# Performance work log

Hardware: AMD Instinct MI355X
Metric: run time of the kernel (lower is better)

Reference implementation:

```python
import jax, jax.numpy as jnp
import numpy as np

B, C_IN, C_OUT, H, W = 16, 64, 64, 256, 256
M1, M2 = 32, 32  # retained Fourier modes (low-frequency corner block)


def setup_inputs() -> dict:
    key = jax.random.key(0)
    kx, kw, kb = jax.random.split(key, 3)
    x = jax.random.normal(kx, (B, C_IN, H, W), dtype=jnp.float32)
    # xavier_uniform over (in, out, m1, m2): fan_in = C_IN*M1*M2, fan_out = C_OUT*M1*M2
    bound = float(np.sqrt(6.0 / ((C_IN + C_OUT) * M1 * M2)))
    weights = jax.random.uniform(kw, (C_IN, C_OUT, M1, M2), jnp.float32, -bound, bound)
    bias = jax.random.normal(kb, (C_OUT,), dtype=jnp.float32) * 0.01
    return {"x": x, "weights": weights, "bias": bias}


def reference(x, weights, bias):
    # x: [B, Cin, H, W] real -> rFFT2 -> [B, Cin, H, W//2+1] complex
    x_ft = jnp.fft.rfft2(x, axes=(-2, -1))
    m1 = min(M1, x_ft.shape[-2])
    m2 = min(M2, x_ft.shape[-1])
    # Single fused complex-times-real channel mixing over the truncated mode block
    mixed = jnp.einsum("bixy,ioxy->boxy",
                       x_ft[:, :, :m1, :m2],
                       weights[:, :, :m1, :m2].astype(x_ft.dtype))
    out_ft = jnp.zeros((x.shape[0], weights.shape[1], x_ft.shape[-2], x_ft.shape[-1]),
                       dtype=x_ft.dtype)
    out_ft = out_ft.at[:, :, :m1, :m2].set(mixed)
    x_out = jnp.fft.irfft2(out_ft, s=(x.shape[-2], x.shape[-1]), axes=(-2, -1))
    return x_out + bias[None, :, None, None]
```

## Files before the change

### kernel.cpp

```cpp
#include <hip/hip_runtime.h>


#define H_ 256
#define W_ 256

typedef short short8 __attribute__((ext_vector_type(8)));
typedef float floatx4 __attribute__((ext_vector_type(4)));

static __device__ __forceinline__ unsigned short f2b(float f) {
    union { float f; unsigned int u; } v; v.f = f;
    unsigned int r = v.u + 0x7FFFu + ((v.u >> 16) & 1u);
    return (unsigned short)(r >> 16);
}

__global__ void build_tables(unsigned short* ws) {
    int k = blockIdx.x;
    int n = threadIdx.x;
    int u = (k * n) & 255;
    double ang = 6.283185307179586476925286766559 * (double)u / 256.0;
    float c = (float)cos(ang), s = (float)sin(ang);
    unsigned short bc = f2b(c), bs = f2b(s), bns = f2b(-s);
    unsigned short* F2t = ws;
    unsigned short* F1e = ws + 16384;
    unsigned short* G1  = ws + 16384 + 32768;
    unsigned short* G2t = ws + 16384 + 65536;

    F2t[(2 * k) * 256 + n]     = bc;
    F2t[(2 * k + 1) * 256 + n] = bns;
    F1e[(2 * k) * 512 + 2 * n]         = bc;
    F1e[(2 * k) * 512 + 2 * n + 1]     = bs;
    F1e[(2 * k + 1) * 512 + 2 * n]     = bns;
    F1e[(2 * k + 1) * 512 + 2 * n + 1] = bc;
    G1[(2 * n) * 64 + 2 * k]         = bc;
    G1[(2 * n) * 64 + 2 * k + 1]     = bns;
    G1[(2 * n + 1) * 64 + 2 * k]     = bs;
    G1[(2 * n + 1) * 64 + 2 * k + 1] = bc;
    float fac = (k == 0) ? 1.f : 2.f;
    G2t[n * 64 + 2 * k]     = f2b(fac * c);
    G2t[n * 64 + 2 * k + 1] = f2b(-fac * s);
}

__global__ __launch_bounds__(256) void fwd_kernel(const float* __restrict__ x,
                                                  const unsigned short* __restrict__ ws_u,
                                                  float* __restrict__ Y) {
    __shared__ __align__(16) unsigned short lT[32 * 520];
    const int tid = threadIdx.x;
    const int wave = tid >> 6, lane = tid & 63;
    const int lm = lane & 15, lq = lane >> 4;
    const int bi = blockIdx.x;

    const float* xg = x + (size_t)bi * (H_ * W_);
    const unsigned short* F2tg = ws_u;
    const unsigned short* F1eg = ws_u + 16384;

    floatx4 acc[4][4];
    for (int a = 0; a < 4; ++a)
        for (int b = 0; b < 4; ++b) acc[a][b] = (floatx4){0.f, 0.f, 0.f, 0.f};

    for (int kc = 0; kc < 4; ++kc) {
        for (int kk = 0; kk < 2; ++kk) {
            short8 af[4], bf[4];
            for (int a = 0; a < 4; ++a) {
                const float* ap = xg + (((wave * 4 + a) * 16 + lm) * 256 + kc * 64 + kk * 32 + lq * 8);
                const float4 v0 = *(const float4*)ap;
                const float4 v1 = *(const float4*)(ap + 4);
                short8 t;
                t[0] = (short)f2b(v0.x); t[1] = (short)f2b(v0.y);
                t[2] = (short)f2b(v0.z); t[3] = (short)f2b(v0.w);
                t[4] = (short)f2b(v1.x); t[5] = (short)f2b(v1.y);
                t[6] = (short)f2b(v1.z); t[7] = (short)f2b(v1.w);
                af[a] = t;
            }
            for (int b = 0; b < 4; ++b)
                bf[b] = *(const short8*)(F2tg + (b * 16 + lm) * 256 + kc * 64 + kk * 32 + lq * 8);
            for (int a = 0; a < 4; ++a)
                for (int b = 0; b < 4; ++b)
                    acc[a][b] = __builtin_amdgcn_mfma_f32_16x16x32_bf16(af[a], bf[b], acc[a][b], 0, 0, 0);
        }
    }
    for (int a = 0; a < 4; ++a) {
        int mbase = (wave * 4 + a) * 16 + lq * 4;
        for (int b = 0; b < 4; ++b) {
            int col = b * 16 + lm;
            int ky = col >> 1, c = col & 1;
            for (int r = 0; r < 4; ++r) {
                int h = mbase + r;
                lT[ky * 520 + 2 * h + c] = f2b(acc[a][b][r]);
            }
        }
    }
    __syncthreads();
    floatx4 acc2[2];
    acc2[0] = (floatx4){0.f, 0.f, 0.f, 0.f};
    acc2[1] = (floatx4){0.f, 0.f, 0.f, 0.f};
    for (int ks = 0; ks < 16; ++ks) {
        short8 af = *(const short8*)(F1eg + (wave * 16 + lm) * 512 + ks * 32 + lq * 8);
        for (int b = 0; b < 2; ++b) {
            short8 bf = *(const short8*)(lT + (b * 16 + lm) * 520 + ks * 32 + lq * 8);
            acc2[b] = __builtin_amdgcn_mfma_f32_16x16x32_bf16(af, bf, acc2[b], 0, 0, 0);
        }
    }
    float* Yg = Y + (size_t)bi * (64 * 32);
    for (int b = 0; b < 2; ++b) {
        int colk = b * 16 + lm;
        int mrow = wave * 16 + lq * 4;
        for (int r = 0; r < 4; ++r)
            Yg[(mrow + r) * 32 + colk] = acc2[b][r];
    }
}

__global__ __launch_bounds__(256) void mix_kernel(const float* __restrict__ Wg,
                                                  const float* __restrict__ Y,
                                                  unsigned short* __restrict__ Mx) {
    __shared__ float lW[64 * 64];
    __shared__ float lY[16 * 130];
    const int tid = threadIdx.x;
    const int bid = blockIdx.x;
    const int mode = (bid & 7) * 128 + (bid >> 3);
    const int kx = mode >> 5, ky = mode & 31;

    for (int q = 0; q < 16; ++q) {
        int e = q * 256 + tid;
        lW[e] = Wg[(size_t)e * 1024 + kx * 32 + ky];
    }
    for (int q = 0; q < 8; ++q) {
        int e = q * 256 + tid;
        int b = e >> 7, r = e & 127;
        lY[b * 130 + r] = Y[(((size_t)b * 64 + (r >> 1)) * 64 + 2 * kx + (r & 1)) * 32 + ky];
    }
    __syncthreads();

    const int og = tid & 7;
    const int bc = tid >> 3;
    const int b = bc >> 1, c = bc & 1;
    float acc[8];
    for (int j = 0; j < 8; ++j) acc[j] = 0.f;
    for (int i = 0; i < 64; ++i) {
        float yv = lY[b * 130 + 2 * i + c];
        const floatx4 w0 = *(const floatx4*)&lW[i * 64 + og * 8];
        const floatx4 w1 = *(const floatx4*)&lW[i * 64 + og * 8 + 4];
        acc[0] += yv * w0[0]; acc[1] += yv * w0[1];
        acc[2] += yv * w0[2]; acc[3] += yv * w0[3];
        acc[4] += yv * w1[0]; acc[5] += yv * w1[1];
        acc[6] += yv * w1[2]; acc[7] += yv * w1[3];
    }
    const float scale = 1.f / 65536.f;
    for (int j = 0; j < 8; ++j) {
        int o = og * 8 + j;
        Mx[((size_t)(b * 64 + o) * 64 + 2 * kx + c) * 32 + ky] = f2b(acc[j] * scale);
    }
}

__global__ __launch_bounds__(256) void inv_kernel(const unsigned short* __restrict__ ws_u,
                                                  const unsigned short* __restrict__ Mx,
                                                  const float* __restrict__ bias,
                                                  float* __restrict__ out) {
    __shared__ __align__(16) unsigned short lMx[32 * 64];
    __shared__ __align__(16) unsigned short lZ[256 * 72];
    const int tid = threadIdx.x;
    const int wave = tid >> 6, lane = tid & 63;
    const int lm = lane & 15, lq = lane >> 4;
    const int bo = blockIdx.x;
    const int o = bo & 63;

    const unsigned short* G1g = ws_u + 49152;
    const unsigned short* G2g = ws_u + 81920;

    {
        short8 v = *(const short8*)(Mx + (size_t)bo * 2048 + tid * 8);
        int kx2 = tid >> 2, kyb = (tid & 3) * 8;
        for (int e = 0; e < 8; ++e)
            lMx[(kyb + e) * 64 + kx2] = (unsigned short)v[e];
    }
    __syncthreads();

    {
        floatx4 accc[8][2];
        for (int a = 0; a < 8; ++a)
            for (int b = 0; b < 2; ++b) accc[a][b] = (floatx4){0.f, 0.f, 0.f, 0.f};
        for (int ks = 0; ks < 2; ++ks) {
            short8 bf[2];
            for (int b = 0; b < 2; ++b)
                bf[b] = *(const short8*)(lMx + (b * 16 + lm) * 64 + ks * 32 + lq * 8);
            for (int a = 0; a < 8; ++a) {
                int mt = wave * 8 + a;
                short8 af = *(const short8*)(G1g + (mt * 16 + lm) * 64 + ks * 32 + lq * 8);
                for (int b = 0; b < 2; ++b)
                    accc[a][b] = __builtin_amdgcn_mfma_f32_16x16x32_bf16(af, bf[b], accc[a][b], 0, 0, 0);
            }
        }
        for (int a = 0; a < 8; ++a) {
            int mbase = (wave * 8 + a) * 16 + lq * 4;
            for (int b = 0; b < 2; ++b) {
                int ky = b * 16 + lm;
                for (int r = 0; r < 4; ++r) {
                    int m = mbase + r;
                    int h = m >> 1, c = m & 1;
                    lZ[h * 72 + 2 * ky + c] = f2b(accc[a][b][r]);
                }
            }
        }
    }
    __syncthreads();

    const float bv = bias[o];
    float* og = out + (size_t)bo * (H_ * W_);
    for (int s = 0; s < 4; ++s) {
        floatx4 accd[4][4];
        for (int a = 0; a < 4; ++a)
            for (int b = 0; b < 4; ++b) accd[a][b] = (floatx4){0.f, 0.f, 0.f, 0.f};
        for (int ks = 0; ks < 2; ++ks) {
            short8 af[4], bf[4];
            for (int a = 0; a < 4; ++a) {
                int mt = s * 4 + a;
                af[a] = *(const short8*)(lZ + (mt * 16 + lm) * 72 + ks * 32 + lq * 8);
            }
            for (int b = 0; b < 4; ++b) {
                int nt = wave * 4 + b;
                bf[b] = *(const short8*)(G2g + (nt * 16 + lm) * 64 + ks * 32 + lq * 8);
            }
            for (int a = 0; a < 4; ++a)
                for (int b = 0; b < 4; ++b)
                    accd[a][b] = __builtin_amdgcn_mfma_f32_16x16x32_bf16(af[a], bf[b], accd[a][b], 0, 0, 0);
        }
        for (int a = 0; a < 4; ++a) {
            int hbase = (s * 4 + a) * 16 + lq * 4;
            for (int b = 0; b < 4; ++b) {
                int w = (wave * 4 + b) * 16 + lm;
                for (int r = 0; r < 4; ++r)
                    og[(hbase + r) * 256 + w] = accd[a][b][r] + bv;
            }
        }
    }
}

extern "C" void kernel_launch(void* const* d_in, const int* in_sizes, int n_in,
                              void* d_out, int out_size, void* d_ws, size_t ws_size,
                              hipStream_t stream) {
    const float* x    = (const float*)d_in[0];
    const float* w    = (const float*)d_in[1];
    const float* bias = (const float*)d_in[2];
    float* out = (float*)d_out;
    unsigned short* ws_u = (unsigned short*)d_ws;
    float* Y = (float*)((char*)d_ws + 196608);
    unsigned short* Mx = (unsigned short*)((char*)d_ws + 8585216);

    build_tables<<<32, 256, 0, stream>>>(ws_u);
    fwd_kernel<<<1024, 256, 0, stream>>>(x, ws_u, Y);
    mix_kernel<<<1024, 256, 0, stream>>>(w, Y, Mx);
    inv_kernel<<<1024, 256, 0, stream>>>(ws_u, Mx, bias, out);
}
```

Baseline: 525.7 us.

## Restructure FFT kernels: coalesced LDS staging, register-cached twiddles, pretransposed weights

```diff
diff --git a/kernel.cpp b/kernel.cpp
--- a/kernel.cpp
+++ b/kernel.cpp
@@ -11,6 +11,12 @@
     union { float f; unsigned int u; } v; v.f = f;
     unsigned int r = v.u + 0x7FFFu + ((v.u >> 16) & 1u);
     return (unsigned short)(r >> 16);
+}
+
+static __device__ __forceinline__ unsigned int cvt_pk_bf16(float a, float b) {
+    unsigned int r;
+    asm("v_cvt_pk_bf16_f32 %0, %1, %2" : "=v"(r) : "v"(a), "v"(b));
+    return r;
 }
 
 __global__ void build_tables(unsigned short* ws) {
@@ -40,9 +46,29 @@
     G2t[n * 64 + 2 * k + 1] = f2b(-fac * s);
 }
 
-__global__ __launch_bounds__(256) void fwd_kernel(const float* __restrict__ x,
-                                                  const unsigned short* __restrict__ ws_u,
-                                                  float* __restrict__ Y) {
+__global__ __launch_bounds__(256) void wtrans(const float* __restrict__ Wg,
+                                              float* __restrict__ Wt) {
+    __shared__ float t[64][65];
+    const int iot = blockIdx.x;
+    const int mt = blockIdx.y;
+    const int tid = threadIdx.x;
+    for (int q = 0; q < 16; ++q) {
+        int idx = q * 256 + tid;
+        int io = idx >> 6, m = idx & 63;
+        t[io][m] = Wg[(size_t)(iot * 64 + io) * 1024 + mt * 64 + m];
+    }
+    __syncthreads();
+    for (int q = 0; q < 16; ++q) {
+        int idx = q * 256 + tid;
+        int m = idx >> 6, io = idx & 63;
+        Wt[(size_t)(mt * 64 + m) * 4096 + iot * 64 + io] = t[io][m];
+    }
+}
+
+__global__ __launch_bounds__(256, 2) void fwd_kernel(const float* __restrict__ x,
+                                                     const unsigned short* __restrict__ ws_u,
+                                                     float* __restrict__ Y) {
+    __shared__ __align__(16) unsigned short lA[64 * 264];
     __shared__ __align__(16) unsigned short lT[32 * 520];
     const int tid = threadIdx.x;
     const int wave = tid >> 6, lane = tid & 63;
@@ -53,39 +79,44 @@
     const unsigned short* F2tg = ws_u;
     const unsigned short* F1eg = ws_u + 16384;
 
-    floatx4 acc[4][4];
-    for (int a = 0; a < 4; ++a)
-        for (int b = 0; b < 4; ++b) acc[a][b] = (floatx4){0.f, 0.f, 0.f, 0.f};
-
-    for (int kc = 0; kc < 4; ++kc) {
-        for (int kk = 0; kk < 2; ++kk) {
-            short8 af[4], bf[4];
-            for (int a = 0; a < 4; ++a) {
-                const float* ap = xg + (((wave * 4 + a) * 16 + lm) * 256 + kc * 64 + kk * 32 + lq * 8);
-                const float4 v0 = *(const float4*)ap;
-                const float4 v1 = *(const float4*)(ap + 4);
-                short8 t;
-                t[0] = (short)f2b(v0.x); t[1] = (short)f2b(v0.y);
-                t[2] = (short)f2b(v0.z); t[3] = (short)f2b(v0.w);
-                t[4] = (short)f2b(v1.x); t[5] = (short)f2b(v1.y);
-                t[6] = (short)f2b(v1.z); t[7] = (short)f2b(v1.w);
-                af[a] = t;
-            }
+    short8 bfA[8][4];
+#pragma unroll
+    for (int kk = 0; kk < 8; ++kk)
+#pragma unroll
+        for (int b = 0; b < 4; ++b)
+            bfA[kk][b] = *(const short8*)(F2tg + (b * 16 + lm) * 256 + kk * 32 + lq * 8);
+
+    floatx4 acc[4];
+    for (int hc = 0; hc < 4; ++hc) {
+        if (hc) __syncthreads();
+#pragma unroll
+        for (int j = 0; j < 16; ++j) {
+            int fi = j * 256 + tid;
+            int row = fi >> 6, c4 = fi & 63;
+            const float4 v = *(const float4*)(xg + (hc * 64 + row) * 256 + c4 * 4);
+            uint2 p;
+            p.x = cvt_pk_bf16(v.x, v.y);
+            p.y = cvt_pk_bf16(v.z, v.w);
+            *(uint2*)(lA + row * 264 + c4 * 4) = p;
+        }
+        __syncthreads();
+#pragma unroll
+        for (int b = 0; b < 4; ++b) acc[b] = (floatx4){0.f, 0.f, 0.f, 0.f};
+#pragma unroll
+        for (int kk = 0; kk < 8; ++kk) {
+            short8 af = *(const short8*)(lA + (wave * 16 + lm) * 264 + kk * 32 + lq * 8);
+#pragma unroll
             for (int b = 0; b < 4; ++b)
-                bf[b] = *(const short8*)(F2tg + (b * 16 + lm) * 256 + kc * 64 + kk * 32 + lq * 8);
-            for (int a = 0; a < 4; ++a)
-                for (int b = 0; b < 4; ++b)
-                    acc[a][b] = __builtin_amdgcn_mfma_f32_16x16x32_bf16(af[a], bf[b], acc[a][b], 0, 0, 0);
-        }
-    }
-    for (int a = 0; a < 4; ++a) {
-        int mbase = (wave * 4 + a) * 16 + lq * 4;
+                acc[b] = __builtin_amdgcn_mfma_f32_16x16x32_bf16(af, bfA[kk][b], acc[b], 0, 0, 0);
+        }
+#pragma unroll
         for (int b = 0; b < 4; ++b) {
             int col = b * 16 + lm;
             int ky = col >> 1, c = col & 1;
+#pragma unroll
             for (int r = 0; r < 4; ++r) {
-                int h = mbase + r;
-                lT[ky * 520 + 2 * h + c] = f2b(acc[a][b][r]);
+                int h = hc * 64 + wave * 16 + lq * 4 + r;
+                lT[ky * 520 + 2 * h + c] = f2b(acc[b][r]);
             }
         }
     }
@@ -95,21 +126,24 @@
     acc2[1] = (floatx4){0.f, 0.f, 0.f, 0.f};
     for (int ks = 0; ks < 16; ++ks) {
         short8 af = *(const short8*)(F1eg + (wave * 16 + lm) * 512 + ks * 32 + lq * 8);
+#pragma unroll
         for (int b = 0; b < 2; ++b) {
             short8 bf = *(const short8*)(lT + (b * 16 + lm) * 520 + ks * 32 + lq * 8);
             acc2[b] = __builtin_amdgcn_mfma_f32_16x16x32_bf16(af, bf, acc2[b], 0, 0, 0);
         }
     }
     float* Yg = Y + (size_t)bi * (64 * 32);
+#pragma unroll
     for (int b = 0; b < 2; ++b) {
         int colk = b * 16 + lm;
         int mrow = wave * 16 + lq * 4;
+#pragma unroll
         for (int r = 0; r < 4; ++r)
             Yg[(mrow + r) * 32 + colk] = acc2[b][r];
     }
 }
 
-__global__ __launch_bounds__(256) void mix_kernel(const float* __restrict__ Wg,
+__global__ __launch_bounds__(256) void mix_kernel(const float* __restrict__ Wt,
                                                   const float* __restrict__ Y,
                                                   unsigned short* __restrict__ Mx) {
     __shared__ float lW[64 * 64];
@@ -119,9 +153,10 @@
     const int mode = (bid & 7) * 128 + (bid >> 3);
     const int kx = mode >> 5, ky = mode & 31;
 
-    for (int q = 0; q < 16; ++q) {
-        int e = q * 256 + tid;
-        lW[e] = Wg[(size_t)e * 1024 + kx * 32 + ky];
+    {
+        const float4* src = (const float4*)(Wt + (size_t)mode * 4096);
+        float4* dst = (float4*)lW;
+        for (int q = 0; q < 4; ++q) dst[q * 256 + tid] = src[q * 256 + tid];
     }
     for (int q = 0; q < 8; ++q) {
         int e = q * 256 + tid;
@@ -134,6 +169,7 @@
     const int bc = tid >> 3;
     const int b = bc >> 1, c = bc & 1;
     float acc[8];
+#pragma unroll
     for (int j = 0; j < 8; ++j) acc[j] = 0.f;
     for (int i = 0; i < 64; ++i) {
         float yv = lY[b * 130 + 2 * i + c];
@@ -145,18 +181,20 @@
         acc[6] += yv * w1[2]; acc[7] += yv * w1[3];
     }
     const float scale = 1.f / 65536.f;
+#pragma unroll
     for (int j = 0; j < 8; ++j) {
         int o = og * 8 + j;
         Mx[((size_t)(b * 64 + o) * 64 + 2 * kx + c) * 32 + ky] = f2b(acc[j] * scale);
     }
 }
 
-__global__ __launch_bounds__(256) void inv_kernel(const unsigned short* __restrict__ ws_u,
-                                                  const unsigned short* __restrict__ Mx,
-                                                  const float* __restrict__ bias,
-                                                  float* __restrict__ out) {
+__global__ __launch_bounds__(256, 2) void inv_kernel(const unsigned short* __restrict__ ws_u,
+                                                     const unsigned short* __restrict__ Mx,
+                                                     const float* __restrict__ bias,
+                                                     float* __restrict__ out) {
     __shared__ __align__(16) unsigned short lMx[32 * 64];
     __shared__ __align__(16) unsigned short lZ[256 * 72];
+    __shared__ __align__(16) float lOut[32 * 260];
     const int tid = threadIdx.x;
     const int wave = tid >> 6, lane = tid & 63;
     const int lm = lane & 15, lq = lane >> 4;
@@ -165,10 +203,19 @@
 
     const unsigned short* G1g = ws_u + 49152;
     const unsigned short* G2g = ws_u + 81920;
+    const float bv = bias[o];
+
+    short8 bfD[2][4];
+#pragma unroll
+    for (int ks = 0; ks < 2; ++ks)
+#pragma unroll
+        for (int b = 0; b < 4; ++b)
+            bfD[ks][b] = *(const short8*)(G2g + ((wave * 4 + b) * 16 + lm) * 64 + ks * 32 + lq * 8);
 
     {
         short8 v = *(const short8*)(Mx + (size_t)bo * 2048 + tid * 8);
         int kx2 = tid >> 2, kyb = (tid & 3) * 8;
+#pragma unroll
         for (int e = 0; e < 8; ++e)
             lMx[(kyb + e) * 64 + kx2] = (unsigned short)v[e];
     }
@@ -176,23 +223,32 @@
 
     {
         floatx4 accc[8][2];
+#pragma unroll
         for (int a = 0; a < 8; ++a)
+#pragma unroll
             for (int b = 0; b < 2; ++b) accc[a][b] = (floatx4){0.f, 0.f, 0.f, 0.f};
+#pragma unroll
         for (int ks = 0; ks < 2; ++ks) {
             short8 bf[2];
+#pragma unroll
             for (int b = 0; b < 2; ++b)
                 bf[b] = *(const short8*)(lMx + (b * 16 + lm) * 64 + ks * 32 + lq * 8);
+#pragma unroll
             for (int a = 0; a < 8; ++a) {
                 int mt = wave * 8 + a;
                 short8 af = *(const short8*)(G1g + (mt * 16 + lm) * 64 + ks * 32 + lq * 8);
+#pragma unroll
                 for (int b = 0; b < 2; ++b)
                     accc[a][b] = __builtin_amdgcn_mfma_f32_16x16x32_bf16(af, bf[b], accc[a][b], 0, 0, 0);
             }
         }
+#pragma unroll
         for (int a = 0; a < 8; ++a) {
             int mbase = (wave * 8 + a) * 16 + lq * 4;
+#pragma unroll
             for (int b = 0; b < 2; ++b) {
                 int ky = b * 16 + lm;
+#pragma unroll
                 for (int r = 0; r < 4; ++r) {
                     int m = mbase + r;
                     int h = m >> 1, c = m & 1;
@@ -203,32 +259,48 @@
     }
     __syncthreads();
 
-    const float bv = bias[o];
     float* og = out + (size_t)bo * (H_ * W_);
     for (int s = 0; s < 4; ++s) {
         floatx4 accd[4][4];
+#pragma unroll
         for (int a = 0; a < 4; ++a)
+#pragma unroll
             for (int b = 0; b < 4; ++b) accd[a][b] = (floatx4){0.f, 0.f, 0.f, 0.f};
+#pragma unroll
         for (int ks = 0; ks < 2; ++ks) {
-            short8 af[4], bf[4];
+            short8 af[4];
+#pragma unroll
             for (int a = 0; a < 4; ++a) {
                 int mt = s * 4 + a;
                 af[a] = *(const short8*)(lZ + (mt * 16 + lm) * 72 + ks * 32 + lq * 8);
             }
-            for (int b = 0; b < 4; ++b) {
-                int nt = wave * 4 + b;
-                bf[b] = *(const short8*)(G2g + (nt * 16 + lm) * 64 + ks * 32 + lq * 8);
-            }
+#pragma unroll
             for (int a = 0; a < 4; ++a)
+#pragma unroll
                 for (int b = 0; b < 4; ++b)
-                    accd[a][b] = __builtin_amdgcn_mfma_f32_16x16x32_bf16(af[a], bf[b], accd[a][b], 0, 0, 0);
-        }
-        for (int a = 0; a < 4; ++a) {
-            int hbase = (s * 4 + a) * 16 + lq * 4;
-            for (int b = 0; b < 4; ++b) {
-                int w = (wave * 4 + b) * 16 + lm;
-                for (int r = 0; r < 4; ++r)
-                    og[(hbase + r) * 256 + w] = accd[a][b][r] + bv;
+                    accd[a][b] = __builtin_amdgcn_mfma_f32_16x16x32_bf16(af[a], bfD[ks][b], accd[a][b], 0, 0, 0);
+        }
+        for (int g = 0; g < 2; ++g) {
+            __syncthreads();
+#pragma unroll
+            for (int a2 = 0; a2 < 2; ++a2) {
+                int a = g * 2 + a2;
+#pragma unroll
+                for (int b = 0; b < 4; ++b) {
+                    int col = wave * 64 + b * 16 + lm;
+#pragma unroll
+                    for (int r = 0; r < 4; ++r) {
+                        int row = a2 * 16 + lq * 4 + r;
+                        lOut[row * 260 + col] = accd[a][b][r] + bv;
+                    }
+                }
+            }
+            __syncthreads();
+#pragma unroll
+            for (int j = 0; j < 8; ++j) {
+                int row = wave * 8 + j;
+                floatx4 v = *(const floatx4*)(lOut + row * 260 + lane * 4);
+                *(floatx4*)(og + (s * 64 + g * 32 + row) * 256 + lane * 4) = v;
             }
         }
     }
@@ -242,11 +314,13 @@
     const float* bias = (const float*)d_in[2];
     float* out = (float*)d_out;
     unsigned short* ws_u = (unsigned short*)d_ws;
-    float* Y = (float*)((char*)d_ws + 196608);
+    float* Y  = (float*)((char*)d_ws + 196608);
     unsigned short* Mx = (unsigned short*)((char*)d_ws + 8585216);
+    float* Wt = (float*)((char*)d_ws + 33554432);
 
     build_tables<<<32, 256, 0, stream>>>(ws_u);
+    wtrans<<<dim3(64, 16), 256, 0, stream>>>(w, Wt);
     fwd_kernel<<<1024, 256, 0, stream>>>(x, ws_u, Y);
-    mix_kernel<<<1024, 256, 0, stream>>>(w, Y, Mx);
+    mix_kernel<<<1024, 256, 0, stream>>>(Wt, Y, Mx);
     inv_kernel<<<1024, 256, 0, stream>>>(ws_u, Mx, bias, out);
 }
```

Measured after the change: 505.3 us. 1.04x faster.
